# Kernel tuning notes

Hardware: AMD Instinct MI355X
Metric: run time of the kernel (lower is better)

The kernel has to match this reference:

```python
import jax, jax.numpy as jnp
import numpy as np

NUM_NEG = 100
TEMP = 0.05
EPS = 1e-12  # matches F.normalize eps


def _l2norm(x):
    n = jnp.sqrt(jnp.sum(x * x, axis=-1, keepdims=True))
    return x / jnp.maximum(n, EPS)


def setup_inputs() -> dict:
    key = jax.random.key(0)
    k1, k2, k3, k4, k5, k6 = jax.random.split(key, 6)
    B, S, D = 1024, 50, 64
    NUM_ITEMS = 100000  # table has NUM_ITEMS+1 rows (row 0 = padding)
    N = B * S
    return {
        "output_embeddings": jax.random.normal(k1, (B, S, D), dtype=jnp.float32),
        "target_ids": jax.random.randint(k2, (B, S), 1, NUM_ITEMS + 1, dtype=jnp.int64)
                      if jax.config.jax_enable_x64 else
                      jax.random.randint(k2, (B, S), 1, NUM_ITEMS + 1).astype(jnp.int32),
        "all_item_embeddings": jax.random.normal(k3, (NUM_ITEMS + 1, D), dtype=jnp.float32),
        "supervision_weights": jax.random.uniform(k4, (B, S), dtype=jnp.float32),
        "neg_indices": jax.random.randint(k5, (N, NUM_NEG), 1, NUM_ITEMS + 1).astype(jnp.int32),
        "alt_neg_indices": jax.random.randint(k6, (N, NUM_NEG), 1, NUM_ITEMS + 1).astype(jnp.int32),
    }


def reference(output_embeddings, target_ids, all_item_embeddings,
              supervision_weights, neg_indices, alt_neg_indices):
    B, S, D = output_embeddings.shape
    flat_out = output_embeddings.reshape(-1, D)            # [N, D]
    flat_tgt = target_ids.reshape(-1)                       # [N]
    flat_w = supervision_weights.reshape(-1)                # [N]
    valid = flat_w > 0

    vo = _l2norm(flat_out)                                  # [N, D]
    items = _l2norm(all_item_embeddings)                    # [V, D]

    pos_e = items[flat_tgt]                                 # [N, D]
    pos_logit = jnp.sum(vo * pos_e, axis=1)                 # [N]

    # resample negatives that collide with the positive target
    neg = jnp.where(neg_indices != flat_tgt[:, None], neg_indices, alt_neg_indices)
    neg_e = items[neg]                                      # [N, K, D]
    neg_logits = jnp.einsum('nd,nkd->nk', vo, neg_e)        # [N, K]

    logits = jnp.concatenate([pos_logit[:, None], neg_logits], axis=1) / TEMP
    # cross-entropy with label 0 == logsumexp - positive logit
    loss_per = jax.nn.logsumexp(logits, axis=1) - logits[:, 0]

    wm = jnp.where(valid, flat_w, 0.0)
    return jnp.sum(loss_per * wm) / jnp.sum(wm)
```

## Files before the change

### kernel.cpp

```cpp
#include <hip/hip_runtime.h>


#define D_DIM 64
#define K_NEG 100
#define INV_TEMP 20.0f
#define MAX_LOGIT 20.0f
#define LOG2E 1.4426950408889634f
#define LN2 0.6931471805599453f
#define MAXL2 28.853900817779268f
#define MCONST (INV_TEMP / (127.0f * 127.0f))
#define MC2 (MCONST * LOG2E)

#define NBLK_MAIN 2048
#define NBLK_QNT 1024

typedef float fv4 __attribute__((ext_vector_type(4)));
typedef unsigned int uv4 __attribute__((ext_vector_type(4)));

__device__ __forceinline__ int DOT4(int a, int b, int c) {
#if __has_builtin(__builtin_amdgcn_sdot4)
  return __builtin_amdgcn_sdot4(a, b, c, false);
#else
  int r = c;
#pragma unroll
  for (int i = 0; i < 4; ++i)
    r += (int)(signed char)(a >> (8 * i)) * (int)(signed char)(b >> (8 * i));
  return r;
#endif
}

__device__ __forceinline__ unsigned int pack8(const fv4 x, float s) {
  const int b0 = (int)rintf(x.x * s) & 255;
  const int b1 = (int)rintf(x.y * s) & 255;
  const int b2 = (int)rintf(x.z * s) & 255;
  const int b3 = (int)rintf(x.w * s) & 255;
  return (unsigned)b0 | ((unsigned)b1 << 8) | ((unsigned)b2 << 16) |
         ((unsigned)b3 << 24);
}

__global__ __launch_bounds__(256) void quantize_kernel(
    const float* __restrict__ items, unsigned int* __restrict__ tab8, int V,
    const float* __restrict__ oe, unsigned int* __restrict__ q8, int N) {
  const int lane = threadIdx.x & 63;
  const int wid  = threadIdx.x >> 6;
  const int g = lane >> 4, q = lane & 15;
  const int waveId = blockIdx.x * 4 + wid;
  const int nWaves = gridDim.x * 4;
  for (int base = waveId * 4; base < V; base += nWaves * 4) {
    const int r = base + g;
    const bool act = (r < V);
    fv4 x = {0.f, 0.f, 0.f, 0.f};
    if (act) x = *reinterpret_cast<const fv4*>(items + (size_t)r * D_DIM + q * 4);
    float ss = x.x * x.x + x.y * x.y + x.z * x.z + x.w * x.w;
    ss += __shfl_xor(ss, 1);
    ss += __shfl_xor(ss, 2);
    ss += __shfl_xor(ss, 4);
    ss += __shfl_xor(ss, 8);
    const float s = 127.0f / fmaxf(sqrtf(ss), 1e-12f);
    if (act) tab8[(size_t)r * 16 + q] = pack8(x, s);
  }
  for (int base = waveId * 4; base < N; base += nWaves * 4) {
    const int r = base + g;
    const bool act = (r < N);
    fv4 x = {0.f, 0.f, 0.f, 0.f};
    if (act) x = *reinterpret_cast<const fv4*>(oe + (size_t)r * D_DIM + q * 4);
    float ss = x.x * x.x + x.y * x.y + x.z * x.z + x.w * x.w;
    ss += __shfl_xor(ss, 1);
    ss += __shfl_xor(ss, 2);
    ss += __shfl_xor(ss, 4);
    ss += __shfl_xor(ss, 8);
    const float s = 127.0f / fmaxf(sqrtf(ss), 1e-12f);
    if (act) q8[(size_t)r * 16 + q] = pack8(x, s);
  }
}

__global__ __launch_bounds__(256) void loss_kernel(
    const unsigned int* __restrict__ q8,
    const int*   __restrict__ tgt,
    const unsigned int* __restrict__ tab8,
    const float* __restrict__ wgt,
    const int*   __restrict__ negi,
    const int*   __restrict__ alti,
    float2*      __restrict__ partials,
    int N) {
  __shared__ float2 s_red[4];
  const int lane = threadIdx.x & 63;
  const int wid  = threadIdx.x >> 6;
  const int waveId = blockIdx.x * 4 + wid;
  const int nWaves = gridDim.x * 4;
  const bool v1ok = (lane <= K_NEG - 64);

  float num = 0.f, den = 0.f;

  int row = waveId;
  int t_r = 0, n0 = 0, n1 = 0;
  float w = 0.f;
  if (row < N) {
    t_r = tgt[row];
    w = wgt[row];
    const int* nr = negi + (size_t)row * K_NEG;
    if (lane >= 1) n0 = nr[lane - 1];
    if (v1ok) n1 = nr[63 + lane];
  }

  while (row < N) {
    const int nxt = row + nWaves;

    const int* ar = alti + (size_t)row * K_NEG;
    int i0 = (lane == 0) ? t_r : n0;
    if (lane >= 1 && i0 == t_r) i0 = ar[lane - 1];
    int i1 = v1ok ? n1 : 0;
    if (v1ok && i1 == t_r) i1 = ar[63 + lane];

    const uv4* t0 = reinterpret_cast<const uv4*>(tab8 + ((unsigned)i0 << 4));
    const uv4* t1 = reinterpret_cast<const uv4*>(tab8 + ((unsigned)i1 << 4));
    const uv4 a0 = t0[0], a1 = t0[1], a2 = t0[2], a3 = t0[3];
    const uv4 b0 = t1[0], b1 = t1[1], b2 = t1[2], b3 = t1[3];
    const uv4* qp = reinterpret_cast<const uv4*>(q8 + (size_t)row * 16);
    const uv4 q0 = qp[0], q1 = qp[1], q2 = qp[2], q3 = qp[3];

    int p_t = 0, pn0 = 0, pn1 = 0;
    float p_w = 0.f;
    if (nxt < N) {
      p_t = tgt[nxt];
      p_w = wgt[nxt];
      const int* nr = negi + (size_t)nxt * K_NEG;
      if (lane >= 1) pn0 = __builtin_nontemporal_load(nr + lane - 1);
      if (v1ok) pn1 = __builtin_nontemporal_load(nr + 63 + lane);
    }

    int d0 = 0, d1 = 0;
    d0 = DOT4((int)a0.x, (int)q0.x, d0);
    d1 = DOT4((int)b0.x, (int)q0.x, d1);
    d0 = DOT4((int)a0.y, (int)q0.y, d0);
    d1 = DOT4((int)b0.y, (int)q0.y, d1);
    d0 = DOT4((int)a0.z, (int)q0.z, d0);
    d1 = DOT4((int)b0.z, (int)q0.z, d1);
    d0 = DOT4((int)a0.w, (int)q0.w, d0);
    d1 = DOT4((int)b0.w, (int)q0.w, d1);
    d0 = DOT4((int)a1.x, (int)q1.x, d0);
    d1 = DOT4((int)b1.x, (int)q1.x, d1);
    d0 = DOT4((int)a1.y, (int)q1.y, d0);
    d1 = DOT4((int)b1.y, (int)q1.y, d1);
    d0 = DOT4((int)a1.z, (int)q1.z, d0);
    d1 = DOT4((int)b1.z, (int)q1.z, d1);
    d0 = DOT4((int)a1.w, (int)q1.w, d0);
    d1 = DOT4((int)b1.w, (int)q1.w, d1);
    d0 = DOT4((int)a2.x, (int)q2.x, d0);
    d1 = DOT4((int)b2.x, (int)q2.x, d1);
    d0 = DOT4((int)a2.y, (int)q2.y, d0);
    d1 = DOT4((int)b2.y, (int)q2.y, d1);
    d0 = DOT4((int)a2.z, (int)q2.z, d0);
    d1 = DOT4((int)b2.z, (int)q2.z, d1);
    d0 = DOT4((int)a2.w, (int)q2.w, d0);
    d1 = DOT4((int)b2.w, (int)q2.w, d1);
    d0 = DOT4((int)a3.x, (int)q3.x, d0);
    d1 = DOT4((int)b3.x, (int)q3.x, d1);
    d0 = DOT4((int)a3.y, (int)q3.y, d0);
    d1 = DOT4((int)b3.y, (int)q3.y, d1);
    d0 = DOT4((int)a3.z, (int)q3.z, d0);
    d1 = DOT4((int)b3.z, (int)q3.z, d1);
    d0 = DOT4((int)a3.w, (int)q3.w, d0);
    d1 = DOT4((int)b3.w, (int)q3.w, d1);

    float e = exp2f(fmaf((float)d0, MC2, -MAXL2));
    if (v1ok) e += exp2f(fmaf((float)d1, MC2, -MAXL2));

    e += __shfl_xor(e, 1);
    e += __shfl_xor(e, 2);
    e += __shfl_xor(e, 4);
    e += __shfl_xor(e, 8);
    e += __shfl_xor(e, 16);
    e += __shfl_xor(e, 32);
    if (lane == 0) {
      const float pos = (float)d0 * MCONST;
      const float lse = log2f(e) * LN2 + MAX_LOGIT;
      const float loss = lse - pos;
      if (w > 0.f) {
        num += loss * w;
        den += w;
      }
    }

    t_r = p_t; n0 = pn0; n1 = pn1; w = p_w;
    row = nxt;
  }

  if (lane == 0) s_red[wid] = make_float2(num, den);
  __syncthreads();
  if (threadIdx.x == 0) {
    float n = 0.f, d = 0.f;
#pragma unroll
    for (int i = 0; i < 4; ++i) { n += s_red[i].x; d += s_red[i].y; }
    partials[blockIdx.x] = make_float2(n, d);
  }
}

__global__ __launch_bounds__(256) void finish_kernel(
    const float2* __restrict__ partials, int nblk, float* __restrict__ out) {
  float num = 0.f, den = 0.f;
  for (int i = threadIdx.x; i < nblk; i += 256) {
    const float2 p = partials[i];
    num += p.x;
    den += p.y;
  }
#pragma unroll
  for (int m = 1; m < 64; m <<= 1) {
    num += __shfl_xor(num, m);
    den += __shfl_xor(den, m);
  }
  __shared__ float2 red[4];
  const int wid = threadIdx.x >> 6;
  const int lane = threadIdx.x & 63;
  if (lane == 0) red[wid] = make_float2(num, den);
  __syncthreads();
  if (threadIdx.x == 0) {
    float n = 0.f, d = 0.f;
#pragma unroll
    for (int i = 0; i < 4; ++i) { n += red[i].x; d += red[i].y; }
    out[0] = n / d;
  }
}

extern "C" void kernel_launch(void* const* d_in, const int* in_sizes, int n_in,
                              void* d_out, int out_size, void* d_ws, size_t ws_size,
                              hipStream_t stream) {
  const float* oe    = (const float*)d_in[0];
  const int*   tgt   = (const int*)  d_in[1];
  const float* items = (const float*)d_in[2];
  const float* wgt   = (const float*)d_in[3];
  const int*   negi  = (const int*)  d_in[4];
  const int*   alti  = (const int*)  d_in[5];

  const int N = in_sizes[0] / D_DIM;
  const int V = in_sizes[2] / D_DIM;

  unsigned int* tab8 = (unsigned int*)d_ws;
  size_t off = ((size_t)V * 64 + 255) & ~(size_t)255;
  unsigned int* q8 = (unsigned int*)((char*)d_ws + off);
  size_t off2 = (off + (size_t)N * 64 + 255) & ~(size_t)255;
  float2* partials = (float2*)((char*)d_ws + off2);

  quantize_kernel<<<NBLK_QNT, 256, 0, stream>>>(items, tab8, V, oe, q8, N);
  loss_kernel<<<NBLK_MAIN, 256, 0, stream>>>(q8, tgt, tab8, wgt, negi, alti,
                                             partials, N);
  finish_kernel<<<1, 256, 0, stream>>>(partials, NBLK_MAIN, (float*)d_out);
}
```

Baseline: 72.73 us.

## Split int8 item table into halves processed by two cache-friendly gather passes

Splits the quantized item table into two halves holding the first and last 32 dimensions, each about 3.2 MB. Two passes then compute the dot products: the first writes 16-bit partial sums per row, and the second adds the remaining half and computes the loss. The aim is to keep each half-table resident in cache during the random gathers. In exchange, the negative and alt indices are read twice and a partial-sum buffer (N*256 bytes) is written and read back, which adds traffic and a kernel launch.

```diff
diff --git a/kernel.cpp b/kernel.cpp
--- a/kernel.cpp
+++ b/kernel.cpp
@@ -39,7 +39,8 @@
 }
 
 __global__ __launch_bounds__(256) void quantize_kernel(
-    const float* __restrict__ items, unsigned int* __restrict__ tab8, int V,
+    const float* __restrict__ items, unsigned int* __restrict__ tabA,
+    unsigned int* __restrict__ tabB, int V,
     const float* __restrict__ oe, unsigned int* __restrict__ q8, int N) {
   const int lane = threadIdx.x & 63;
   const int wid  = threadIdx.x >> 6;
@@ -57,7 +58,11 @@
     ss += __shfl_xor(ss, 4);
     ss += __shfl_xor(ss, 8);
     const float s = 127.0f / fmaxf(sqrtf(ss), 1e-12f);
-    if (act) tab8[(size_t)r * 16 + q] = pack8(x, s);
+    if (act) {
+      const unsigned int u = pack8(x, s);
+      if (q < 8) tabA[(size_t)r * 8 + q] = u;
+      else       tabB[(size_t)r * 8 + (q - 8)] = u;
+    }
   }
   for (int base = waveId * 4; base < N; base += nWaves * 4) {
     const int r = base + g;
@@ -74,30 +79,23 @@
   }
 }
 
-__global__ __launch_bounds__(256) void loss_kernel(
+__global__ __launch_bounds__(256) void partA_kernel(
     const unsigned int* __restrict__ q8,
     const int*   __restrict__ tgt,
-    const unsigned int* __restrict__ tab8,
-    const float* __restrict__ wgt,
+    const unsigned int* __restrict__ tabA,
     const int*   __restrict__ negi,
     const int*   __restrict__ alti,
-    float2*      __restrict__ partials,
+    unsigned int* __restrict__ part,
     int N) {
-  __shared__ float2 s_red[4];
   const int lane = threadIdx.x & 63;
-  const int wid  = threadIdx.x >> 6;
-  const int waveId = blockIdx.x * 4 + wid;
+  const int waveId = blockIdx.x * 4 + (threadIdx.x >> 6);
   const int nWaves = gridDim.x * 4;
   const bool v1ok = (lane <= K_NEG - 64);
 
-  float num = 0.f, den = 0.f;
-
   int row = waveId;
   int t_r = 0, n0 = 0, n1 = 0;
-  float w = 0.f;
   if (row < N) {
     t_r = tgt[row];
-    w = wgt[row];
     const int* nr = negi + (size_t)row * K_NEG;
     if (lane >= 1) n0 = nr[lane - 1];
     if (v1ok) n1 = nr[63 + lane];
@@ -112,18 +110,16 @@
     int i1 = v1ok ? n1 : 0;
     if (v1ok && i1 == t_r) i1 = ar[63 + lane];
 
-    const uv4* t0 = reinterpret_cast<const uv4*>(tab8 + ((unsigned)i0 << 4));
-    const uv4* t1 = reinterpret_cast<const uv4*>(tab8 + ((unsigned)i1 << 4));
-    const uv4 a0 = t0[0], a1 = t0[1], a2 = t0[2], a3 = t0[3];
-    const uv4 b0 = t1[0], b1 = t1[1], b2 = t1[2], b3 = t1[3];
+    const uv4* t0 = reinterpret_cast<const uv4*>(tabA + ((size_t)(unsigned)i0 << 3));
+    const uv4* t1 = reinterpret_cast<const uv4*>(tabA + ((size_t)(unsigned)i1 << 3));
+    const uv4 a0 = t0[0], a1 = t0[1];
+    const uv4 b0 = t1[0], b1 = t1[1];
     const uv4* qp = reinterpret_cast<const uv4*>(q8 + (size_t)row * 16);
-    const uv4 q0 = qp[0], q1 = qp[1], q2 = qp[2], q3 = qp[3];
+    const uv4 q0 = qp[0], q1 = qp[1];
 
     int p_t = 0, pn0 = 0, pn1 = 0;
-    float p_w = 0.f;
     if (nxt < N) {
       p_t = tgt[nxt];
-      p_w = wgt[nxt];
       const int* nr = negi + (size_t)nxt * K_NEG;
       if (lane >= 1) pn0 = __builtin_nontemporal_load(nr + lane - 1);
       if (v1ok) pn1 = __builtin_nontemporal_load(nr + 63 + lane);
@@ -146,22 +142,92 @@
     d1 = DOT4((int)b1.z, (int)q1.z, d1);
     d0 = DOT4((int)a1.w, (int)q1.w, d0);
     d1 = DOT4((int)b1.w, (int)q1.w, d1);
-    d0 = DOT4((int)a2.x, (int)q2.x, d0);
-    d1 = DOT4((int)b2.x, (int)q2.x, d1);
-    d0 = DOT4((int)a2.y, (int)q2.y, d0);
-    d1 = DOT4((int)b2.y, (int)q2.y, d1);
-    d0 = DOT4((int)a2.z, (int)q2.z, d0);
-    d1 = DOT4((int)b2.z, (int)q2.z, d1);
-    d0 = DOT4((int)a2.w, (int)q2.w, d0);
-    d1 = DOT4((int)b2.w, (int)q2.w, d1);
-    d0 = DOT4((int)a3.x, (int)q3.x, d0);
-    d1 = DOT4((int)b3.x, (int)q3.x, d1);
-    d0 = DOT4((int)a3.y, (int)q3.y, d0);
-    d1 = DOT4((int)b3.y, (int)q3.y, d1);
-    d0 = DOT4((int)a3.z, (int)q3.z, d0);
-    d1 = DOT4((int)b3.z, (int)q3.z, d1);
-    d0 = DOT4((int)a3.w, (int)q3.w, d0);
-    d1 = DOT4((int)b3.w, (int)q3.w, d1);
+
+    const unsigned int pu = ((unsigned)(unsigned short)(short)d0) |
+                            (((unsigned)(unsigned short)(short)d1) << 16);
+    __builtin_nontemporal_store(pu, part + (size_t)row * 64 + lane);
+
+    t_r = p_t; n0 = pn0; n1 = pn1;
+    row = nxt;
+  }
+}
+
+__global__ __launch_bounds__(256) void loss_kernel(
+    const unsigned int* __restrict__ q8,
+    const int*   __restrict__ tgt,
+    const unsigned int* __restrict__ tabB,
+    const float* __restrict__ wgt,
+    const int*   __restrict__ negi,
+    const int*   __restrict__ alti,
+    const unsigned int* __restrict__ part,
+    float2*      __restrict__ partials,
+    int N) {
+  __shared__ float2 s_red[4];
+  const int lane = threadIdx.x & 63;
+  const int wid  = threadIdx.x >> 6;
+  const int waveId = blockIdx.x * 4 + wid;
+  const int nWaves = gridDim.x * 4;
+  const bool v1ok = (lane <= K_NEG - 64);
+
+  float num = 0.f, den = 0.f;
+
+  int row = waveId;
+  int t_r = 0, n0 = 0, n1 = 0;
+  float w = 0.f;
+  if (row < N) {
+    t_r = tgt[row];
+    w = wgt[row];
+    const int* nr = negi + (size_t)row * K_NEG;
+    if (lane >= 1) n0 = nr[lane - 1];
+    if (v1ok) n1 = nr[63 + lane];
+  }
+
+  while (row < N) {
+    const int nxt = row + nWaves;
+
+    const int* ar = alti + (size_t)row * K_NEG;
+    int i0 = (lane == 0) ? t_r : n0;
+    if (lane >= 1 && i0 == t_r) i0 = ar[lane - 1];
+    int i1 = v1ok ? n1 : 0;
+    if (v1ok && i1 == t_r) i1 = ar[63 + lane];
+
+    const uv4* t0 = reinterpret_cast<const uv4*>(tabB + ((size_t)(unsigned)i0 << 3));
+    const uv4* t1 = reinterpret_cast<const uv4*>(tabB + ((size_t)(unsigned)i1 << 3));
+    const uv4 a0 = t0[0], a1 = t0[1];
+    const uv4 b0 = t1[0], b1 = t1[1];
+    const uv4* qp = reinterpret_cast<const uv4*>(q8 + (size_t)row * 16);
+    const uv4 q0 = qp[2], q1 = qp[3];
+    const unsigned int pu =
+        __builtin_nontemporal_load(part + (size_t)row * 64 + lane);
+
+    int p_t = 0, pn0 = 0, pn1 = 0;
+    float p_w = 0.f;
+    if (nxt < N) {
+      p_t = tgt[nxt];
+      p_w = wgt[nxt];
+      const int* nr = negi + (size_t)nxt * K_NEG;
+      if (lane >= 1) pn0 = __builtin_nontemporal_load(nr + lane - 1);
+      if (v1ok) pn1 = __builtin_nontemporal_load(nr + 63 + lane);
+    }
+
+    int d0 = (int)(short)(pu & 0xffffu);
+    int d1 = (int)(short)(pu >> 16);
+    d0 = DOT4((int)a0.x, (int)q0.x, d0);
+    d1 = DOT4((int)b0.x, (int)q0.x, d1);
+    d0 = DOT4((int)a0.y, (int)q0.y, d0);
+    d1 = DOT4((int)b0.y, (int)q0.y, d1);
+    d0 = DOT4((int)a0.z, (int)q0.z, d0);
+    d1 = DOT4((int)b0.z, (int)q0.z, d1);
+    d0 = DOT4((int)a0.w, (int)q0.w, d0);
+    d1 = DOT4((int)b0.w, (int)q0.w, d1);
+    d0 = DOT4((int)a1.x, (int)q1.x, d0);
+    d1 = DOT4((int)b1.x, (int)q1.x, d1);
+    d0 = DOT4((int)a1.y, (int)q1.y, d0);
+    d1 = DOT4((int)b1.y, (int)q1.y, d1);
+    d0 = DOT4((int)a1.z, (int)q1.z, d0);
+    d1 = DOT4((int)b1.z, (int)q1.z, d1);
+    d0 = DOT4((int)a1.w, (int)q1.w, d0);
+    d1 = DOT4((int)b1.w, (int)q1.w, d1);
 
     float e = exp2f(fmaf((float)d0, MC2, -MAXL2));
     if (v1ok) e += exp2f(fmaf((float)d1, MC2, -MAXL2));
@@ -235,14 +301,19 @@
   const int N = in_sizes[0] / D_DIM;
   const int V = in_sizes[2] / D_DIM;
 
-  unsigned int* tab8 = (unsigned int*)d_ws;
+  unsigned int* tabA = (unsigned int*)d_ws;
+  unsigned int* tabB = tabA + (size_t)V * 8;
   size_t off = ((size_t)V * 64 + 255) & ~(size_t)255;
   unsigned int* q8 = (unsigned int*)((char*)d_ws + off);
   size_t off2 = (off + (size_t)N * 64 + 255) & ~(size_t)255;
-  float2* partials = (float2*)((char*)d_ws + off2);
-
-  quantize_kernel<<<NBLK_QNT, 256, 0, stream>>>(items, tab8, V, oe, q8, N);
-  loss_kernel<<<NBLK_MAIN, 256, 0, stream>>>(q8, tgt, tab8, wgt, negi, alti,
-                                             partials, N);
+  unsigned int* part = (unsigned int*)((char*)d_ws + off2);
+  size_t off3 = (off2 + (size_t)N * 256 + 255) & ~(size_t)255;
+  float2* partials = (float2*)((char*)d_ws + off3);
+
+  quantize_kernel<<<NBLK_QNT, 256, 0, stream>>>(items, tabA, tabB, V, oe, q8, N);
+  partA_kernel<<<NBLK_MAIN, 256, 0, stream>>>(q8, tgt, tabA, negi, alti,
+                                              part, N);
+  loss_kernel<<<NBLK_MAIN, 256, 0, stream>>>(q8, tgt, tabB, wgt, negi, alti,
+                                             part, partials, N);
   finish_kernel<<<1, 256, 0, stream>>>(partials, NBLK_MAIN, (float*)d_out);
 }
```

Result: slower. 100.2 us (+37.7%).
